# Kernel optimization log

Measured on AMD Instinct MI355X. Metric: run time of the kernel, lower is better.

## Reference

```python
import jax, jax.numpy as jnp
import numpy as np

TAU_M = 0.01
TAU_I = 0.005
DT = 0.001
ALPHA = float(np.exp(-DT / TAU_M))  # applied to current (as in source)
BETA = float(np.exp(-DT / TAU_I))   # applied to voltage (as in source)

B, T, N, NI = 16, 1000, 4096, 1024


def setup_inputs() -> dict:
    key = jax.random.key(0)
    k0, k1, k2, k3 = jax.random.split(key, 4)
    neuron_types = jnp.where(jax.random.uniform(k0, (N,)) < 0.8, 1, -1).astype(jnp.int32)
    recurrent_weights = (jax.random.normal(k1, (N, N), jnp.float32) / np.sqrt(N)).astype(jnp.float32)
    feedforward_weights = (jax.random.normal(k2, (N, NI), jnp.float32) / np.sqrt(NI)).astype(jnp.float32)
    inputs = (jax.random.uniform(k3, (B, T, NI)) < 0.05).astype(jnp.float32)
    return {
        "initial_v": jnp.zeros((B, N), jnp.float32),
        "initial_I": jnp.zeros((B, N), jnp.float32),
        "inputs": inputs,
        "recurrent_weights": recurrent_weights,
        "feedforward_weights": feedforward_weights,
        "E_weight": jnp.asarray(1.0, jnp.float32),
        "I_weight": jnp.asarray(1.0, jnp.float32),
        "E_v_th": jnp.asarray(1.0, jnp.float32),
        "I_v_th": jnp.asarray(1.0, jnp.float32),
        "neuron_types": neuron_types,
        "n_steps": T,
    }


def reference(initial_v, initial_I, inputs, recurrent_weights, feedforward_weights,
              E_weight, I_weight, E_v_th, I_v_th, neuron_types, n_steps):
    exc = neuron_types == 1
    # per-column scaling, exactly as source: W * scale[None, :]
    scaled_w = recurrent_weights * jnp.where(exc, E_weight, I_weight)[None, :]  # (N, N)
    v_th = jnp.where(exc, E_v_th, I_v_th)  # (N,)
    # precomputed feedforward drive, as in source: (B, T, N)
    ff = jnp.einsum("bti,ni->btn", inputs, feedforward_weights)
    # NOTE: source initializes s = zeros and never updates it in the loop,
    # so the recurrent term s @ scaled_w is identically zero. Replicated faithfully.
    s = jnp.zeros_like(initial_v)  # (B, N)

    def step(carry, ff_t):
        v, cur = carry
        cur = ALPHA * cur + ff_t + s @ scaled_w
        v = BETA * v + cur - s
        spikes = (v >= v_th[None, :]).astype(v.dtype)
        v = v * (1.0 - spikes)
        return (v, cur), None

    (v, cur), _ = jax.lax.scan(step, (initial_v, initial_I), jnp.swapaxes(ff, 0, 1))
    return (v, cur)
```

## Files before the change

kernel.cpp:

```cpp
#include <hip/hip_runtime.h>
#include <cmath>
#include <cstdint>
#include <cstddef>


typedef _Float16 half8 __attribute__((ext_vector_type(8)));
typedef float floatx4 __attribute__((ext_vector_type(4)));

#define WSCALE 1024.0f
#define WSCALE_INV (1.0f / 1024.0f)

#define VMW4 asm volatile("s_waitcnt vmcnt(4)" ::: "memory")
#define VMW0 asm volatile("s_waitcnt vmcnt(0)" ::: "memory")
#define BAR  __builtin_amdgcn_s_barrier()

__device__ __forceinline__ void gload16(const void* g, void* l) {
    __builtin_amdgcn_global_load_lds(
        (const __attribute__((address_space(1))) unsigned int*)g,
        (__attribute__((address_space(3))) unsigned int*)l, 16, 0, 0);
}

__global__ __launch_bounds__(256) void k_wprep(const float* __restrict__ Wff,
                                               _Float16* __restrict__ Wt2,
                                               int N, int NI) {
    int tid = blockIdx.x * 256 + (int)threadIdx.x;
    int per_row = NI >> 3;
    int n = tid / per_row;
    int ic = (tid - n * per_row) << 3;
    if (n >= N) return;
    const float4* src = (const float4*)(Wff + (size_t)n * NI + ic);
    float4 w0 = src[0], w1 = src[1];
    float wv[8] = {w0.x, w0.y, w0.z, w0.w, w1.x, w1.y, w1.z, w1.w};
    half8 hi, lo;
#pragma unroll
    for (int j = 0; j < 8; ++j) {
        float w = wv[j] * WSCALE;
        _Float16 h = (_Float16)w;
        hi[j] = h;
        lo[j] = (_Float16)(w - (float)h);
    }
    *(half8*)(Wt2 + (size_t)n * (2 * NI) + ic) = hi;
    *(half8*)(Wt2 + (size_t)n * (2 * NI) + NI + ic) = lo;
}

__device__ __forceinline__ void xconv_range(const float* __restrict__ x,
                                            _Float16* __restrict__ X16,
                                            int g0, int gstep, int xrows,
                                            int t0, int tc, int T, int NI) {
    int per_row = NI >> 3;
    int G = xrows * per_row;
    for (int g = g0; g < G; g += gstep) {
        int r = g / per_row;
        int gi = g - r * per_row;
        int b = r / tc;
        int tl = r - b * tc;
        size_t off = ((size_t)(b * T + t0 + tl) * NI) + ((size_t)gi << 3);
        const float4* src = (const float4*)(x + off);
        float4 a = src[0], c = src[1];
        half8 o;
        o[0] = (_Float16)a.x; o[1] = (_Float16)a.y;
        o[2] = (_Float16)a.z; o[3] = (_Float16)a.w;
        o[4] = (_Float16)c.x; o[5] = (_Float16)c.y;
        o[6] = (_Float16)c.z; o[7] = (_Float16)c.w;
        *(half8*)(X16 + off) = o;
    }
}

__global__ __launch_bounds__(256) void k_xpre(const float* __restrict__ x,
                                              _Float16* __restrict__ X16,
                                              int xrows, int t0, int tc,
                                              int T, int NI) {
    xconv_range(x, X16, blockIdx.x * 256 + (int)threadIdx.x,
                (int)gridDim.x * 256, xrows, t0, tc, T, NI);
}

__global__ __launch_bounds__(512, 2) void k_chunk(
    const _Float16* __restrict__ Wt2, const _Float16* __restrict__ X16,
    _Float16* __restrict__ x16w, const float* __restrict__ xin,
    float* __restrict__ ff_dst, const float* __restrict__ ff_src,
    const float* __restrict__ vin, const float* __restrict__ cin,
    float* __restrict__ vout, float* __restrict__ cout,
    const int* __restrict__ ntype, const float* __restrict__ Evth_p,
    const float* __restrict__ Ivth_p,
    int T, int tc_ff, int t0_ff, int tc_rec, int N, int NI,
    float alpha, float beta, int nff, int nrec, int mv,
    int xrows, int t0_x, int tc_x)
{
    __shared__ _Float16 smA[2][2][256 * 32];
    __shared__ _Float16 smB[2][2][256 * 32];
    int blk = blockIdx.x;
    int tid = (int)threadIdx.x;
    if (blk < nff) {
        int Ntiles = N >> 8;
        int mt = blk / Ntiles;
        int nt = blk - mt * Ntiles;
        int m0 = mt << 8, n0 = nt << 8;
        int wid = tid >> 6, lane = tid & 63;
        int wr = wid >> 2, wc = wid & 3;
        int ln15 = lane & 15, kh = lane >> 4;

        int slot4 = (lane & 3) ^ ((lane >> 3) & 3);
        const char* srcA[2]; const char* srcB[2];
        int dB0 = (wid * 2) * 512;
        int dB1 = dB0 + 512;
#pragma unroll
        for (int q = 0; q < 2; ++q) {
            int rl = (wid * 2 + q) * 16 + (lane >> 2);
            int rA = m0 + rl;
            if (rA > mv - 1) rA = mv - 1;
            int b = rA / tc_ff;
            int tl = rA - b * tc_ff;
            srcA[q] = (const char*)(X16 + (size_t)(b * T + t0_ff + tl) * NI + slot4 * 8);
            srcB[q] = (const char*)(Wt2 + (size_t)(n0 + rl) * (2 * NI) + slot4 * 8);
        }
        int amask = NI - 1;

#define STAGE_A(S2, KS, KOFS) { \
        gload16(srcA[0] + (KOFS), &smA[S2][KS][dB0]); \
        gload16(srcA[1] + (KOFS), &smA[S2][KS][dB1]); }
#define STAGE_B(S2, KS, KOFS) { \
        gload16(srcB[0] + (KOFS), &smB[S2][KS][dB0]); \
        gload16(srcB[1] + (KOFS), &smB[S2][KS][dB1]); }

        STAGE_A(0, 0, 0);
        STAGE_B(0, 0, 0);
        STAGE_A(0, 1, 64);
        STAGE_B(0, 1, 64);
        VMW4; BAR;

        int sa  = ((kh ^ ((ln15 >> 1) & 3)) << 3);
        int aro = (wr * 128 + ln15) * 32 + sa;
        int bro = (wc * 64 + ln15) * 32 + sa;

        floatx4 acc[8][4] = {};
        int NKT = (2 * NI) >> 6;

        for (int kt = 0; kt < NKT; ++kt) {
            int s = kt & 1, s2 = s ^ 1;
            bool pre = (kt + 1 < NKT);
            int j64 = (kt + 1) << 6;
            int kA0 = ((j64) & amask) * 2;
            int kA1 = ((j64 + 32) & amask) * 2;
            int kB0 = j64 * 2;
            int kB1 = (j64 + 32) * 2;
            half8 a[4], b[4];
#pragma unroll
            for (int f = 0; f < 4; ++f) b[f] = *(const half8*)(&smB[s][0][bro + f * 512]);
#pragma unroll
            for (int f = 0; f < 4; ++f) a[f] = *(const half8*)(&smA[s][0][aro + f * 512]);
            if (pre) STAGE_A(s2, 0, kA0);
            BAR;
            __builtin_amdgcn_s_setprio(1);
#pragma unroll
            for (int fi = 0; fi < 4; ++fi)
#pragma unroll
                for (int fj = 0; fj < 4; ++fj)
                    acc[fi][fj] = __builtin_amdgcn_mfma_f32_16x16x32_f16(a[fi], b[fj], acc[fi][fj], 0, 0, 0);
            __builtin_amdgcn_s_setprio(0);
            BAR;
#pragma unroll
            for (int f = 0; f < 4; ++f) a[f] = *(const half8*)(&smA[s][0][aro + 2048 + f * 512]);
            if (pre) { STAGE_B(s2, 0, kB0); VMW4; } else { VMW0; }
            BAR;
            __builtin_amdgcn_s_setprio(1);
#pragma unroll
            for (int fi = 0; fi < 4; ++fi)
#pragma unroll
                for (int fj = 0; fj < 4; ++fj)
                    acc[4 + fi][fj] = __builtin_amdgcn_mfma_f32_16x16x32_f16(a[fi], b[fj], acc[4 + fi][fj], 0, 0, 0);
            __builtin_amdgcn_s_setprio(0);
            BAR;
#pragma unroll
            for (int f = 0; f < 4; ++f) b[f] = *(const half8*)(&smB[s][1][bro + f * 512]);
#pragma unroll
            for (int f = 0; f < 4; ++f) a[f] = *(const half8*)(&smA[s][1][aro + f * 512]);
            if (pre) STAGE_A(s2, 1, kA1);
            BAR;
            __builtin_amdgcn_s_setprio(1);
#pragma unroll
            for (int fi = 0; fi < 4; ++fi)
#pragma unroll
                for (int fj = 0; fj < 4; ++fj)
                    acc[fi][fj] = __builtin_amdgcn_mfma_f32_16x16x32_f16(a[fi], b[fj], acc[fi][fj], 0, 0, 0);
            __builtin_amdgcn_s_setprio(0);
            BAR;
#pragma unroll
            for (int f = 0; f < 4; ++f) a[f] = *(const half8*)(&smA[s][1][aro + 2048 + f * 512]);
            if (pre) { STAGE_B(s2, 1, kB1); VMW4; }
            BAR;
            __builtin_amdgcn_s_setprio(1);
#pragma unroll
            for (int fi = 0; fi < 4; ++fi)
#pragma unroll
                for (int fj = 0; fj < 4; ++fj)
                    acc[4 + fi][fj] = __builtin_amdgcn_mfma_f32_16x16x32_f16(a[fi], b[fj], acc[4 + fi][fj], 0, 0, 0);
            __builtin_amdgcn_s_setprio(0);
            BAR;
        }
#undef STAGE_A
#undef STAGE_B
#pragma unroll
        for (int ai = 0; ai < 8; ++ai) {
            int r0 = m0 + wr * 128 + (ai >> 2) * 64 + (ai & 3) * 16 + kh * 4;
#pragma unroll
            for (int fj = 0; fj < 4; ++fj) {
                int nn = n0 + wc * 64 + fj * 16 + ln15;
                float* p = ff_dst + (size_t)r0 * N + nn;
#pragma unroll
                for (int e = 0; e < 4; ++e)
                    if (r0 + e < mv) p[(size_t)e * N] = acc[ai][fj][e] * WSCALE_INV;
            }
        }
    } else if (blk < nff + nrec) {
        int r = (blk - nff) * 512 + tid;
        int e0 = r << 3;
        int b = e0 / N;
        int n = e0 - b * N;
        float vth[8], v[8], cu[8];
#pragma unroll
        for (int j = 0; j < 8; ++j) vth[j] = (ntype[n + j] == 1) ? Evth_p[0] : Ivth_p[0];
        {
            float4 a0 = *(const float4*)(vin + e0), a1 = *(const float4*)(vin + e0 + 4);
            float4 b0 = *(const float4*)(cin + e0), b1 = *(const float4*)(cin + e0 + 4);
            v[0]=a0.x; v[1]=a0.y; v[2]=a0.z; v[3]=a0.w; v[4]=a1.x; v[5]=a1.y; v[6]=a1.z; v[7]=a1.w;
            cu[0]=b0.x; cu[1]=b0.y; cu[2]=b0.z; cu[3]=b0.w; cu[4]=b1.x; cu[5]=b1.y; cu[6]=b1.z; cu[7]=b1.w;
        }
        const float* f = ff_src + (size_t)b * tc_rec * N + n;

#define ST1(J, X) \
        cu[J] = __fadd_rn(__fmul_rn(alpha, cu[J]), (X)); \
        v[J]  = __fadd_rn(__fmul_rn(beta, v[J]), cu[J]); \
        v[J]  = (v[J] >= vth[J]) ? 0.0f : v[J];
#define STEP8(A, Bq) { \
        ST1(0, (A).x) ST1(1, (A).y) ST1(2, (A).z) ST1(3, (A).w) \
        ST1(4, (Bq).x) ST1(5, (Bq).y) ST1(6, (Bq).z) ST1(7, (Bq).w) }

        int t = 0;
        if (tc_rec >= 8) {
            float4 Xa[4], Xb[4], Ya[4], Yb[4];
#pragma unroll
            for (int k = 0; k < 4; ++k) {
                Xa[k] = *(const float4*)(f + (size_t)k * N);
                Xb[k] = *(const float4*)(f + (size_t)k * N + 4);
            }
            for (t = 0; t + 8 <= tc_rec; t += 4) {
#pragma unroll
                for (int k = 0; k < 4; ++k) {
                    Ya[k] = *(const float4*)(f + (size_t)(t + 4 + k) * N);
                    Yb[k] = *(const float4*)(f + (size_t)(t + 4 + k) * N + 4);
                }
#pragma unroll
                for (int k = 0; k < 4; ++k) { STEP8(Xa[k], Xb[k]) }
#pragma unroll
                for (int k = 0; k < 4; ++k) { Xa[k] = Ya[k]; Xb[k] = Yb[k]; }
            }
#pragma unroll
            for (int k = 0; k < 4; ++k) { STEP8(Xa[k], Xb[k]) }
            t += 4;
        }
        for (; t < tc_rec; ++t) {
            float4 a = *(const float4*)(f + (size_t)t * N);
            float4 bq = *(const float4*)(f + (size_t)t * N + 4);
            STEP8(a, bq)
        }
#undef STEP8
#undef ST1
        {
            float4 o0 = {v[0], v[1], v[2], v[3]}, o1 = {v[4], v[5], v[6], v[7]};
            float4 o2 = {cu[0], cu[1], cu[2], cu[3]}, o3 = {cu[4], cu[5], cu[6], cu[7]};
            *(float4*)(vout + e0) = o0; *(float4*)(vout + e0 + 4) = o1;
            *(float4*)(cout + e0) = o2; *(float4*)(cout + e0 + 4) = o3;
        }
    } else {
        int xb = blk - nff - nrec;
        int nxb = (int)gridDim.x - nff - nrec;
        xconv_range(xin, x16w, xb * 512 + tid, nxb * 512,
                    xrows, t0_x, tc_x, T, NI);
    }
}

extern "C" void kernel_launch(void* const* d_in, const int* in_sizes, int n_in,
                              void* d_out, int out_size, void* d_ws, size_t ws_size,
                              hipStream_t stream) {
    const float* initial_v = (const float*)d_in[0];
    const float* initial_I = (const float*)d_in[1];
    const float* inputs    = (const float*)d_in[2];
    const float* Wff       = (const float*)d_in[4];
    const float* Evth      = (const float*)d_in[7];
    const float* Ivth      = (const float*)d_in[8];
    const int*   ntype     = (const int*)d_in[9];

    const int N  = in_sizes[9];
    const int B  = in_sizes[0] / N;
    const int NI = in_sizes[4] / N;
    const int T  = in_sizes[2] / (B * NI);

    char* ws = (char*)d_ws;
    _Float16* Wt2 = (_Float16*)ws;
    size_t wt_b  = (size_t)N * 2 * NI * sizeof(_Float16);
    _Float16* X16 = (_Float16*)(ws + wt_b);
    size_t x_b   = (size_t)B * T * NI * sizeof(_Float16);
    float* state = (float*)(ws + wt_b + x_b);
    size_t st_b  = (size_t)2 * B * N * sizeof(float);
    char*  ffbase = ws + wt_b + x_b + st_b;
    size_t fixed  = wt_b + x_b + st_b;

    size_t avail = (ws_size > fixed) ? (ws_size - fixed) : 0;
    size_t per_t = (size_t)B * N * sizeof(float);
    int TC = (int)(avail / (2 * per_t));
    if (TC > 224) TC = 224;
    if (TC > T) TC = T;
    TC &= ~7;
    if (TC < 8) TC = 8;

    float* fbuf[2];
    fbuf[0] = (float*)ffbase;
    fbuf[1] = (float*)(ffbase + (size_t)TC * per_t);

    const float alpha = (float)exp(-0.001 / 0.01);
    const float beta  = (float)exp(-0.001 / 0.005);

    float* st_v = state;
    float* st_c = state + (size_t)B * N;

    static const int MAXCH = 1024;
    int t0s[MAXCH], tcs[MAXCH];
    int nch = 0;
    {
        int t0 = 0;
        int head = (TC >= 48) ? 48 : TC;
        if (head > T) head = T;
        t0s[nch] = 0; tcs[nch] = head; ++nch; t0 = head;
        while (t0 < T && nch < MAXCH) {
            int rem = T - t0;
            int tc;
            if (rem > TC + 48) {
                tc = TC;
            } else if (rem > 96) {
                tc = rem - 48;
            } else {
                tc = rem;
            }
            if (tc > TC) tc = TC;
            t0s[nch] = t0; tcs[nch] = tc;
            t0 += tc; ++nch;
        }
    }

    k_wprep<<<dim3((N * NI / 8 + 255) / 256), 256, 0, stream>>>(Wff, Wt2, N, NI);
    k_xpre<<<dim3(384), 256, 0, stream>>>(inputs, X16, B * tcs[0], 0, tcs[0], T, NI);

    for (int k = 0; k <= nch; ++k) {
        int tc_ff  = (k < nch) ? tcs[k] : 0;
        int t0_ff  = (k < nch) ? t0s[k] : 0;
        int tc_rec = (k >= 1) ? tcs[k - 1] : 0;
        int nrec   = (k >= 1) ? (B * N) / (512 * 8) : 0;
        int tc_x   = (k + 1 < nch) ? tcs[k + 1] : 0;
        int t0_x   = (k + 1 < nch) ? t0s[k + 1] : 0;
        int nxb    = (tc_x > 0) ? 16 : 0;
        float* ffd = fbuf[k & 1];
        const float* ffs = fbuf[(k ^ 1) & 1];
        const float* vi = (k == 1) ? initial_v : st_v;
        const float* ci = (k == 1) ? initial_I : st_c;
        float* vo = (k == nch) ? (float*)d_out : st_v;
        float* co = (k == nch) ? ((float*)d_out + (size_t)B * N) : st_c;
        int mv  = B * tc_ff;
        int nff = (tc_ff > 0) ? (((mv + 255) >> 8) * (N >> 8)) : 0;
        int grid = nff + nrec + nxb;
        if (grid == 0) continue;
        k_chunk<<<dim3(grid), 512, 0, stream>>>(Wt2, X16, X16, inputs, ffd, ffs,
                                                vi, ci, vo, co,
                                                ntype, Evth, Ivth,
                                                T, tc_ff, t0_ff, tc_rec, N, NI,
                                                alpha, beta, nff, nrec, mv,
                                                B * tc_x, t0_x, tc_x);
    }
}
```

Measured before the change: 525.9 us.

## Halve per-thread recurrence width, deepen prefetch, simplify time chunking

The recurrence blocks now process 4 neurons per thread instead of 8, doubling the number of recurrence blocks to expose more parallelism for the serial time scan. Prefetch depth along time is raised from 4 to 8 steps of float4 loads. The time-chunking schedule drops the small 48-step head chunk and the balanced tail, using uniform chunks capped at 208 and aligned to 16. This adds more blocks competing with the feedforward GEMM blocks, and removing the short head chunk may lengthen the non-overlapped startup.

```diff
diff --git a/kernel.cpp b/kernel.cpp
--- a/kernel.cpp
+++ b/kernel.cpp
@@ -213,17 +213,17 @@
         }
     } else if (blk < nff + nrec) {
         int r = (blk - nff) * 512 + tid;
-        int e0 = r << 3;
+        int e0 = r << 2;
         int b = e0 / N;
         int n = e0 - b * N;
-        float vth[8], v[8], cu[8];
-#pragma unroll
-        for (int j = 0; j < 8; ++j) vth[j] = (ntype[n + j] == 1) ? Evth_p[0] : Ivth_p[0];
+        float vth[4], v[4], cu[4];
+#pragma unroll
+        for (int j = 0; j < 4; ++j) vth[j] = (ntype[n + j] == 1) ? Evth_p[0] : Ivth_p[0];
         {
-            float4 a0 = *(const float4*)(vin + e0), a1 = *(const float4*)(vin + e0 + 4);
-            float4 b0 = *(const float4*)(cin + e0), b1 = *(const float4*)(cin + e0 + 4);
-            v[0]=a0.x; v[1]=a0.y; v[2]=a0.z; v[3]=a0.w; v[4]=a1.x; v[5]=a1.y; v[6]=a1.z; v[7]=a1.w;
-            cu[0]=b0.x; cu[1]=b0.y; cu[2]=b0.z; cu[3]=b0.w; cu[4]=b1.x; cu[5]=b1.y; cu[6]=b1.z; cu[7]=b1.w;
+            float4 a0 = *(const float4*)(vin + e0);
+            float4 b0 = *(const float4*)(cin + e0);
+            v[0]=a0.x; v[1]=a0.y; v[2]=a0.z; v[3]=a0.w;
+            cu[0]=b0.x; cu[1]=b0.y; cu[2]=b0.z; cu[3]=b0.w;
         }
         const float* f = ff_src + (size_t)b * tc_rec * N + n;
 
@@ -231,45 +231,36 @@
         cu[J] = __fadd_rn(__fmul_rn(alpha, cu[J]), (X)); \
         v[J]  = __fadd_rn(__fmul_rn(beta, v[J]), cu[J]); \
         v[J]  = (v[J] >= vth[J]) ? 0.0f : v[J];
-#define STEP8(A, Bq) { \
-        ST1(0, (A).x) ST1(1, (A).y) ST1(2, (A).z) ST1(3, (A).w) \
-        ST1(4, (Bq).x) ST1(5, (Bq).y) ST1(6, (Bq).z) ST1(7, (Bq).w) }
+#define STEP4(A) { ST1(0, (A).x) ST1(1, (A).y) ST1(2, (A).z) ST1(3, (A).w) }
 
         int t = 0;
-        if (tc_rec >= 8) {
-            float4 Xa[4], Xb[4], Ya[4], Yb[4];
-#pragma unroll
-            for (int k = 0; k < 4; ++k) {
-                Xa[k] = *(const float4*)(f + (size_t)k * N);
-                Xb[k] = *(const float4*)(f + (size_t)k * N + 4);
+        if (tc_rec >= 16) {
+            float4 X[8], Y[8];
+#pragma unroll
+            for (int k = 0; k < 8; ++k) X[k] = *(const float4*)(f + (size_t)k * N);
+            for (t = 0; t + 16 <= tc_rec; t += 8) {
+#pragma unroll
+                for (int k = 0; k < 8; ++k) Y[k] = *(const float4*)(f + (size_t)(t + 8 + k) * N);
+#pragma unroll
+                for (int k = 0; k < 8; ++k) { STEP4(X[k]) }
+#pragma unroll
+                for (int k = 0; k < 8; ++k) X[k] = Y[k];
             }
-            for (t = 0; t + 8 <= tc_rec; t += 4) {
-#pragma unroll
-                for (int k = 0; k < 4; ++k) {
-                    Ya[k] = *(const float4*)(f + (size_t)(t + 4 + k) * N);
-                    Yb[k] = *(const float4*)(f + (size_t)(t + 4 + k) * N + 4);
-                }
-#pragma unroll
-                for (int k = 0; k < 4; ++k) { STEP8(Xa[k], Xb[k]) }
-#pragma unroll
-                for (int k = 0; k < 4; ++k) { Xa[k] = Ya[k]; Xb[k] = Yb[k]; }
-            }
-#pragma unroll
-            for (int k = 0; k < 4; ++k) { STEP8(Xa[k], Xb[k]) }
-            t += 4;
+#pragma unroll
+            for (int k = 0; k < 8; ++k) { STEP4(X[k]) }
+            t += 8;
         }
         for (; t < tc_rec; ++t) {
             float4 a = *(const float4*)(f + (size_t)t * N);
-            float4 bq = *(const float4*)(f + (size_t)t * N + 4);
-            STEP8(a, bq)
-        }
-#undef STEP8
+            STEP4(a)
+        }
+#undef STEP4
 #undef ST1
         {
-            float4 o0 = {v[0], v[1], v[2], v[3]}, o1 = {v[4], v[5], v[6], v[7]};
-            float4 o2 = {cu[0], cu[1], cu[2], cu[3]}, o3 = {cu[4], cu[5], cu[6], cu[7]};
-            *(float4*)(vout + e0) = o0; *(float4*)(vout + e0 + 4) = o1;
-            *(float4*)(cout + e0) = o2; *(float4*)(cout + e0 + 4) = o3;
+            float4 o0 = {v[0], v[1], v[2], v[3]};
+            float4 o1 = {cu[0], cu[1], cu[2], cu[3]};
+            *(float4*)(vout + e0) = o0;
+            *(float4*)(cout + e0) = o1;
         }
     } else {
         int xb = blk - nff - nrec;
@@ -308,10 +299,10 @@
     size_t avail = (ws_size > fixed) ? (ws_size - fixed) : 0;
     size_t per_t = (size_t)B * N * sizeof(float);
     int TC = (int)(avail / (2 * per_t));
-    if (TC > 224) TC = 224;
+    if (TC > 208) TC = 208;
     if (TC > T) TC = T;
-    TC &= ~7;
-    if (TC < 8) TC = 8;
+    TC &= ~15;
+    if (TC < 16) TC = 16;
 
     float* fbuf[2];
     fbuf[0] = (float*)ffbase;
@@ -328,19 +319,8 @@
     int nch = 0;
     {
         int t0 = 0;
-        int head = (TC >= 48) ? 48 : TC;
-        if (head > T) head = T;
-        t0s[nch] = 0; tcs[nch] = head; ++nch; t0 = head;
         while (t0 < T && nch < MAXCH) {
-            int rem = T - t0;
-            int tc;
-            if (rem > TC + 48) {
-                tc = TC;
-            } else if (rem > 96) {
-                tc = rem - 48;
-            } else {
-                tc = rem;
-            }
+            int tc = T - t0;
             if (tc > TC) tc = TC;
             t0s[nch] = t0; tcs[nch] = tc;
             t0 += tc; ++nch;
@@ -354,7 +334,7 @@
         int tc_ff  = (k < nch) ? tcs[k] : 0;
         int t0_ff  = (k < nch) ? t0s[k] : 0;
         int tc_rec = (k >= 1) ? tcs[k - 1] : 0;
-        int nrec   = (k >= 1) ? (B * N) / (512 * 8) : 0;
+        int nrec   = (k >= 1) ? (B * N) / (512 * 4) : 0;
         int tc_x   = (k + 1 < nch) ? tcs[k + 1] : 0;
         int t0_x   = (k + 1 < nch) ? t0s[k + 1] : 0;
         int nxb    = (tc_x > 0) ? 16 : 0;
```

Measured after the change: 476.6 us. -9.4%, faster.
